# Optimization experiments

Hardware: AMD Instinct MI355X
Metric: run time of the kernel (lower is better)

Reference implementation:

```python
import jax, jax.numpy as jnp
import numpy as np

L = 64        # label_size = len(label2id)
START = 62    # label2id['START']
STOP = 63     # label2id['STOP']
T = 200000    # sequence length
NEG = -10000.0


def setup_inputs() -> dict:
    key = jax.random.key(0)
    k1, k2 = jax.random.split(key)
    lstm_feats = jax.random.normal(k1, (1, T, L), dtype=jnp.float32)
    transitions = jax.random.normal(k2, (L, L), dtype=jnp.float32)
    # CRF constructor masks: cannot transition INTO START, cannot transition FROM STOP
    transitions = transitions.at[START, :].set(NEG).at[:, STOP].set(NEG)
    return {"lstm_feats": lstm_feats, "transitions": transitions}


def reference(lstm_feats, transitions):
    # Viterbi decode, vectorized over tags; lax.scan over time replaces the
    # nested Python loops of the original (same recurrence, same math).
    feats = lstm_feats[0]  # (T, L)
    init = jnp.full((L,), NEG, dtype=lstm_feats.dtype).at[START].set(0.0)

    def step(v, feat):
        # scores[next, prev] = v[prev] + transitions[next, prev]
        scores = v[None, :] + transitions          # (L, L)
        bp = jnp.argmax(scores, axis=1).astype(jnp.int32)  # backpointers per next_tag
        v_new = jnp.max(scores, axis=1) + feat     # viterbi vars + emission
        return v_new, bp

    v, bptrs = jax.lax.scan(step, init, feats)     # bptrs: (T, L)

    terminal = v + transitions[STOP]               # (L,)
    best = jnp.argmax(terminal).astype(jnp.int32)
    path_score = terminal[best]

    # Backtrack: reverse scan emits the tag chosen at each time step, in order.
    def back(tag, bp):
        return bp[tag], tag

    _, best_path = jax.lax.scan(back, best, bptrs, reverse=True)  # (T,) int32
    return path_score, best_path
```

## Files before the change

kernel.cpp:

```cpp
#include <hip/hip_runtime.h>

#define L 64
#define TLEN 200000
#define CH 528
#define NCH 379
#define LASTLEN (TLEN - (NCH - 1) * CH)
#define MAINT 199992
#define NEGV -10000.0f
#define STARTT 62
#define STOPT 63

#define CKPT_OFF 0
#define M_OFF ((NCH + 1) * L * 4)
#define ETAG_OFF (M_OFF + NCH * L)

typedef float f32x4 __attribute__((ext_vector_type(4)));

#define WAVE_BARRIER() __asm__ volatile("s_waitcnt lgkmcnt(0)\ns_barrier" ::: "memory")
#define STEP_BARRIER() __asm__ volatile("" ::: "memory")

__global__ __launch_bounds__(256, 1) void k_forward(const float* __restrict__ feats,
                                                    const float* __restrict__ trans,
                                                    float* __restrict__ ckpt) {
    const int tid = threadIdx.x;
    const int n = tid & 63;
    const int w = tid >> 6;

    const f32x4* t4 = reinterpret_cast<const f32x4*>(trans) + n * 16 + w * 4;
    f32x4 q0 = t4[0], q1 = t4[1], q2 = t4[2], q3 = t4[3];
    __asm__ volatile("" : "+v"(q0), "+v"(q1), "+v"(q2), "+v"(q3));

    __shared__ __align__(16) float vbuf[3][L];

    vbuf[0][n] = (n == STARTT) ? 0.0f : NEGV;
    vbuf[1][n] = -INFINITY;
    vbuf[2][n] = -INFINITY;
    WAVE_BARRIER();

    float fc[6];
#pragma unroll
    for (int j = 0; j < 6; ++j) fc[j] = feats[j * L + n];

    int nextck = 0, cidx = 0;

#define FWD_STEP(RD, WR, RS, FEAT)                                            \
    do {                                                                      \
        if (w == 0) vbuf[RS][n] = -INFINITY;                                  \
        const f32x4 va0 = *reinterpret_cast<const f32x4*>(&vbuf[RD][16 * w + 0]);  \
        const f32x4 va1 = *reinterpret_cast<const f32x4*>(&vbuf[RD][16 * w + 4]);  \
        const f32x4 va2 = *reinterpret_cast<const f32x4*>(&vbuf[RD][16 * w + 8]);  \
        const f32x4 va3 = *reinterpret_cast<const f32x4*>(&vbuf[RD][16 * w + 12]); \
        const f32x4 s0 = va0 + q0, s1 = va1 + q1, s2 = va2 + q2, s3 = va3 + q3;    \
        const float m0 = fmaxf(fmaxf(s0.x, s0.y), fmaxf(s0.z, s0.w));         \
        const float m1 = fmaxf(fmaxf(s1.x, s1.y), fmaxf(s1.z, s1.w));         \
        const float m2 = fmaxf(fmaxf(s2.x, s2.y), fmaxf(s2.z, s2.w));         \
        const float m3 = fmaxf(fmaxf(s3.x, s3.y), fmaxf(s3.z, s3.w));         \
        const float cand = fmaxf(fmaxf(m0, m1), fmaxf(m2, m3)) + (FEAT);      \
        __hip_atomic_fetch_max(&vbuf[WR][n], cand, __ATOMIC_RELAXED,          \
                               __HIP_MEMORY_SCOPE_WORKGROUP);                 \
        WAVE_BARRIER();                                                       \
    } while (0)

    for (int tb = 0; tb < MAINT; tb += 6) {
        if (tb == nextck) {
            if (w == 0) ckpt[cidx * L + n] = vbuf[0][n];
            nextck += CH;
            ++cidx;
        }
        float fn_[6];
        const bool more = (tb + 6) < MAINT;
        if (more) {
#pragma unroll
            for (int j = 0; j < 6; ++j) fn_[j] = feats[(tb + 6 + j) * L + n];
        }
        FWD_STEP(0, 1, 2, fc[0]);
        FWD_STEP(1, 2, 0, fc[1]);
        FWD_STEP(2, 0, 1, fc[2]);
        FWD_STEP(0, 1, 2, fc[3]);
        FWD_STEP(1, 2, 0, fc[4]);
        FWD_STEP(2, 0, 1, fc[5]);
        if (more) {
#pragma unroll
            for (int j = 0; j < 6; ++j) fc[j] = fn_[j];
        }
    }

    float ft[8];
#pragma unroll
    for (int j = 0; j < 8; ++j) ft[j] = feats[(MAINT + j) * L + n];
    FWD_STEP(0, 1, 2, ft[0]);
    FWD_STEP(1, 2, 0, ft[1]);
    FWD_STEP(2, 0, 1, ft[2]);
    FWD_STEP(0, 1, 2, ft[3]);
    FWD_STEP(1, 2, 0, ft[4]);
    FWD_STEP(2, 0, 1, ft[5]);
    FWD_STEP(0, 1, 2, ft[6]);
    FWD_STEP(1, 2, 0, ft[7]);
    if (w == 0) ckpt[NCH * L + n] = vbuf[2][n];
#undef FWD_STEP
}

__device__ __forceinline__ void load_trow(const float* __restrict__ trans, int n, float* trow) {
#pragma unroll
    for (int i = 0; i < 16; ++i) {
        const f32x4 q = reinterpret_cast<const f32x4*>(trans)[n * 16 + i];
        trow[4 * i + 0] = q.x;
        trow[4 * i + 1] = q.y;
        trow[4 * i + 2] = q.z;
        trow[4 * i + 3] = q.w;
    }
}

__device__ __forceinline__ void replay_chunk(const float* __restrict__ feats,
                                             const float* __restrict__ ckpt,
                                             const float* trow, float* vsh,
                                             unsigned char* bpl, int c, int len, int n) {
    float vreg = ckpt[c * L + n];
    vsh[n] = vreg;
    STEP_BARRIER();
    const int base = c * CH;

    float fc[8];
#pragma unroll
    for (int j = 0; j < 8; ++j) fc[j] = feats[(base + j) * L + n];

    for (int sb = 0; sb < len; sb += 8) {
        float fn_[8];
        const bool more = (sb + 8) < len;
        if (more) {
#pragma unroll
            for (int j = 0; j < 8; ++j) fn_[j] = feats[(base + sb + 8 + j) * L + n];
        }
#pragma unroll
        for (int j = 0; j < 8; ++j) {
            float mc[4];
            int ic[4];
#pragma unroll
            for (int g = 0; g < 4; ++g) {
                float m = -INFINITY;
                int idx = g * 16;
#pragma unroll
                for (int r = 0; r < 4; ++r) {
                    const int pb = g * 16 + r * 4;
                    const f32x4 vv = *reinterpret_cast<const f32x4*>(vsh + pb);
                    const float a = vv.x + trow[pb + 0];
                    const float b = vv.y + trow[pb + 1];
                    const float cc = vv.z + trow[pb + 2];
                    const float d = vv.w + trow[pb + 3];
                    if (a > m)  { m = a;  idx = pb + 0; }
                    if (b > m)  { m = b;  idx = pb + 1; }
                    if (cc > m) { m = cc; idx = pb + 2; }
                    if (d > m)  { m = d;  idx = pb + 3; }
                }
                mc[g] = m;
                ic[g] = idx;
            }
            float m = mc[0];
            int idx = ic[0];
            if (mc[1] > m) { m = mc[1]; idx = ic[1]; }
            if (mc[2] > m) { m = mc[2]; idx = ic[2]; }
            if (mc[3] > m) { m = mc[3]; idx = ic[3]; }

            vreg = m + fc[j];
            bpl[(sb + j) * L + n] = (unsigned char)idx;
            vsh[n] = vreg;
            STEP_BARRIER();
        }
        if (more) {
#pragma unroll
            for (int j = 0; j < 8; ++j) fc[j] = fn_[j];
        }
    }
}

__global__ __launch_bounds__(64, 1) void k_maps(const float* __restrict__ feats,
                                                const float* __restrict__ trans,
                                                const float* __restrict__ ckpt,
                                                unsigned char* __restrict__ M) {
    const int c = blockIdx.x;
    const int n = threadIdx.x;
    const int len = (c == NCH - 1) ? LASTLEN : CH;

    __shared__ __align__(16) float vsh[L];
    __shared__ unsigned char bpl[CH * L];

    float trow[L];
    load_trow(trans, n, trow);
    replay_chunk(feats, ckpt, trow, vsh, bpl, c, len, n);
    __syncthreads();

    int tag = n;
    for (int s = len - 1; s >= 0; --s) tag = bpl[s * L + tag];
    M[c * L + n] = (unsigned char)tag;
}

__global__ __launch_bounds__(64, 1) void k_stitch(const float* __restrict__ trans,
                                                  const float* __restrict__ ckpt,
                                                  const unsigned char* __restrict__ M,
                                                  int* __restrict__ etag,
                                                  float* __restrict__ out) {
    const int n = threadIdx.x;
    __shared__ float tsh[L];
    __shared__ int bsh;
    __shared__ __align__(16) unsigned char msh[NCH * L];

    tsh[n] = ckpt[NCH * L + n] + trans[STOPT * L + n];
    __syncthreads();
    if (n == 0) {
        float m = tsh[0];
        int b = 0;
        for (int p = 1; p < L; ++p)
            if (tsh[p] > m) { m = tsh[p]; b = p; }
        out[0] = m;
        bsh = b;
    }
    __syncthreads();

    for (int i = n; i < (NCH * L) / 4; i += L)
        reinterpret_cast<int*>(msh)[i] = reinterpret_cast<const int*>(M)[i];
    __syncthreads();

    if (n == 0) {
        int carry = bsh;
        for (int c = NCH - 1; c >= 1; --c) {
            etag[c] = carry;
            carry = msh[c * L + carry];
        }
        etag[0] = carry;
    }
}

__global__ __launch_bounds__(64, 1) void k_emit(const float* __restrict__ feats,
                                                const float* __restrict__ trans,
                                                const float* __restrict__ ckpt,
                                                const int* __restrict__ etag,
                                                float* __restrict__ out) {
    const int c = blockIdx.x;
    const int n = threadIdx.x;
    const int len = (c == NCH - 1) ? LASTLEN : CH;

    __shared__ __align__(16) float vsh[L];
    __shared__ unsigned char bpl[CH * L];
    __shared__ unsigned char plc[CH];

    float trow[L];
    load_trow(trans, n, trow);
    replay_chunk(feats, ckpt, trow, vsh, bpl, c, len, n);
    __syncthreads();

    int tag = etag[c];
    for (int s = len - 1; s >= 0; --s) {
        if (n == 0) plc[s] = (unsigned char)tag;
        tag = bpl[s * L + tag];
    }
    __syncthreads();

    for (int i = n; i < len; i += L)
        out[1 + c * CH + i] = (float)plc[i];
}

extern "C" void kernel_launch(void* const* d_in, const int* in_sizes, int n_in,
                              void* d_out, int out_size, void* d_ws, size_t ws_size,
                              hipStream_t stream) {
    const float* feats = (const float*)d_in[0];
    const float* trans = (const float*)d_in[1];
    float* out = (float*)d_out;
    char* ws = (char*)d_ws;
    float* ckpt = (float*)(ws + CKPT_OFF);
    unsigned char* M = (unsigned char*)(ws + M_OFF);
    int* etag = (int*)(ws + ETAG_OFF);

    hipLaunchKernelGGL(k_forward, dim3(1), dim3(256), 0, stream, feats, trans, ckpt);
    hipLaunchKernelGGL(k_maps, dim3(NCH), dim3(64), 0, stream, feats, trans, ckpt, M);
    hipLaunchKernelGGL(k_stitch, dim3(1), dim3(64), 0, stream, trans, ckpt, M, etag, out);
    hipLaunchKernelGGL(k_emit, dim3(NCH), dim3(64), 0, stream, feats, trans, ckpt, etag, out);
}
```

Measured before the change: 33.07 ms.

## Run serial Viterbi forward pass in a single wave without block barriers

The forward max-plus recurrence moves from four waves that combine partial maxima through LDS atomic-max plus s_barrier to a single 64-lane wave that computes the full 64-way max per tag. The first 16 predecessors are taken with readlane broadcasts from registers and the other 48 come from LDS vector reads, reduced with v_max3. This removes the per-step workgroup barrier and the atomic, at the cost of about four times more arithmetic per lane and 64 transition values held in registers. The step unroll goes from 6 to 8, and the separate tail loop is dropped because 8 divides T.

```diff
diff --git a/kernel.cpp b/kernel.cpp
--- a/kernel.cpp
+++ b/kernel.cpp
@@ -5,7 +5,6 @@
 #define CH 528
 #define NCH 379
 #define LASTLEN (TLEN - (NCH - 1) * CH)
-#define MAINT 199992
 #define NEGV -10000.0f
 #define STARTT 62
 #define STOPT 63
@@ -16,87 +15,116 @@
 
 typedef float f32x4 __attribute__((ext_vector_type(4)));
 
-#define WAVE_BARRIER() __asm__ volatile("s_waitcnt lgkmcnt(0)\ns_barrier" ::: "memory")
 #define STEP_BARRIER() __asm__ volatile("" ::: "memory")
 
-__global__ __launch_bounds__(256, 1) void k_forward(const float* __restrict__ feats,
-                                                    const float* __restrict__ trans,
-                                                    float* __restrict__ ckpt) {
-    const int tid = threadIdx.x;
-    const int n = tid & 63;
-    const int w = tid >> 6;
-
-    const f32x4* t4 = reinterpret_cast<const f32x4*>(trans) + n * 16 + w * 4;
-    f32x4 q0 = t4[0], q1 = t4[1], q2 = t4[2], q3 = t4[3];
-    __asm__ volatile("" : "+v"(q0), "+v"(q1), "+v"(q2), "+v"(q3));
-
-    __shared__ __align__(16) float vbuf[3][L];
-
-    vbuf[0][n] = (n == STARTT) ? 0.0f : NEGV;
-    vbuf[1][n] = -INFINITY;
-    vbuf[2][n] = -INFINITY;
-    WAVE_BARRIER();
-
-    float fc[6];
-#pragma unroll
-    for (int j = 0; j < 6; ++j) fc[j] = feats[j * L + n];
+__device__ __forceinline__ float max3f(float a, float b, float c) {
+    float r;
+    __asm__("v_max3_f32 %0, %1, %2, %3" : "=v"(r) : "v"(a), "v"(b), "v"(c));
+    return r;
+}
+__device__ __forceinline__ f32x4 vmax3q(f32x4 a, f32x4 b, f32x4 c) {
+    f32x4 r;
+    r.x = max3f(a.x, b.x, c.x);
+    r.y = max3f(a.y, b.y, c.y);
+    r.z = max3f(a.z, b.z, c.z);
+    r.w = max3f(a.w, b.w, c.w);
+    return r;
+}
+
+#define QC(q, k) ((k) == 0 ? (q).x : ((k) == 1 ? (q).y : ((k) == 2 ? (q).z : (q).w)))
+
+__global__ __launch_bounds__(64, 1) void k_forward(const float* __restrict__ feats,
+                                                   const float* __restrict__ trans,
+                                                   float* __restrict__ ckpt) {
+    const int n = threadIdx.x;
+
+    f32x4 tq[16];
+#pragma unroll
+    for (int i = 0; i < 16; ++i) tq[i] = reinterpret_cast<const f32x4*>(trans)[n * 16 + i];
+
+    __shared__ __align__(16) float vsh[L];
+    const f32x4* vs4 = reinterpret_cast<const f32x4*>(vsh);
+
+    float vreg = (n == STARTT) ? 0.0f : NEGV;
+    vsh[n] = vreg;
+    STEP_BARRIER();
+
+    float fc[8];
+#pragma unroll
+    for (int j = 0; j < 8; ++j) fc[j] = feats[j * L + n];
+
+#define FWD_STEP(FEAT)                                                         \
+    do {                                                                       \
+               \
+        float h[16];                                                           \
+        _Pragma("unroll") for (int p = 0; p < 16; ++p) {                       \
+            const float vp = __int_as_float(                                   \
+                __builtin_amdgcn_readlane(__float_as_int(vreg), p));           \
+            h[p] = vp + QC(tq[p >> 2], p & 3);                                 \
+        }                                                                      \
+        const float a0 = max3f(h[0], h[1], h[2]);                              \
+        const float a1 = max3f(h[3], h[4], h[5]);                              \
+        const float a2 = max3f(h[6], h[7], h[8]);                              \
+        const float a3 = max3f(h[9], h[10], h[11]);                            \
+        const float a4 = max3f(h[12], h[13], h[14]);                           \
+        const float mh = fmaxf(max3f(a0, a1, a2), max3f(a3, a4, h[15]));       \
+              \
+        const f32x4 s4 = vs4[4] + tq[4];                                       \
+        const f32x4 s5 = vs4[5] + tq[5];                                       \
+        const f32x4 s6 = vs4[6] + tq[6];                                       \
+        const f32x4 s7 = vs4[7] + tq[7];                                       \
+        const f32x4 s8 = vs4[8] + tq[8];                                       \
+        const f32x4 s9 = vs4[9] + tq[9];                                       \
+        const f32x4 s10 = vs4[10] + tq[10];                                    \
+        const f32x4 s11 = vs4[11] + tq[11];                                    \
+        const f32x4 s12 = vs4[12] + tq[12];                                    \
+        const f32x4 s13 = vs4[13] + tq[13];                                    \
+        const f32x4 s14 = vs4[14] + tq[14];                                    \
+        const f32x4 s15 = vs4[15] + tq[15];                                    \
+        const f32x4 c0 = vmax3q(s4, s5, s6);                                   \
+        const f32x4 c1 = vmax3q(s7, s8, s9);                                   \
+        const f32x4 c2 = vmax3q(s10, s11, s12);                                \
+        const f32x4 c3 = vmax3q(s13, s14, s15);                                \
+        const f32x4 d0 = vmax3q(c0, c1, c2);                                   \
+        f32x4 e;                                                               \
+        e.x = fmaxf(d0.x, c3.x);                                               \
+        e.y = fmaxf(d0.y, c3.y);                                               \
+        e.z = fmaxf(d0.z, c3.z);                                               \
+        e.w = fmaxf(d0.w, c3.w);                                               \
+        const float m = max3f(max3f(e.x, e.y, e.z), e.w, mh);                  \
+        vreg = m + (FEAT);                                                     \
+        vsh[n] = vreg;                                                         \
+        STEP_BARRIER();                                                        \
+    } while (0)
 
     int nextck = 0, cidx = 0;
 
-#define FWD_STEP(RD, WR, RS, FEAT)                                            \
-    do {                                                                      \
-        if (w == 0) vbuf[RS][n] = -INFINITY;                                  \
-        const f32x4 va0 = *reinterpret_cast<const f32x4*>(&vbuf[RD][16 * w + 0]);  \
-        const f32x4 va1 = *reinterpret_cast<const f32x4*>(&vbuf[RD][16 * w + 4]);  \
-        const f32x4 va2 = *reinterpret_cast<const f32x4*>(&vbuf[RD][16 * w + 8]);  \
-        const f32x4 va3 = *reinterpret_cast<const f32x4*>(&vbuf[RD][16 * w + 12]); \
-        const f32x4 s0 = va0 + q0, s1 = va1 + q1, s2 = va2 + q2, s3 = va3 + q3;    \
-        const float m0 = fmaxf(fmaxf(s0.x, s0.y), fmaxf(s0.z, s0.w));         \
-        const float m1 = fmaxf(fmaxf(s1.x, s1.y), fmaxf(s1.z, s1.w));         \
-        const float m2 = fmaxf(fmaxf(s2.x, s2.y), fmaxf(s2.z, s2.w));         \
-        const float m3 = fmaxf(fmaxf(s3.x, s3.y), fmaxf(s3.z, s3.w));         \
-        const float cand = fmaxf(fmaxf(m0, m1), fmaxf(m2, m3)) + (FEAT);      \
-        __hip_atomic_fetch_max(&vbuf[WR][n], cand, __ATOMIC_RELAXED,          \
-                               __HIP_MEMORY_SCOPE_WORKGROUP);                 \
-        WAVE_BARRIER();                                                       \
-    } while (0)
-
-    for (int tb = 0; tb < MAINT; tb += 6) {
+    for (int tb = 0; tb < TLEN; tb += 8) {
         if (tb == nextck) {
-            if (w == 0) ckpt[cidx * L + n] = vbuf[0][n];
+            ckpt[cidx * L + n] = vreg;
             nextck += CH;
             ++cidx;
         }
-        float fn_[6];
-        const bool more = (tb + 6) < MAINT;
+        float fn_[8];
+        const bool more = (tb + 8) < TLEN;
         if (more) {
 #pragma unroll
-            for (int j = 0; j < 6; ++j) fn_[j] = feats[(tb + 6 + j) * L + n];
-        }
-        FWD_STEP(0, 1, 2, fc[0]);
-        FWD_STEP(1, 2, 0, fc[1]);
-        FWD_STEP(2, 0, 1, fc[2]);
-        FWD_STEP(0, 1, 2, fc[3]);
-        FWD_STEP(1, 2, 0, fc[4]);
-        FWD_STEP(2, 0, 1, fc[5]);
+            for (int j = 0; j < 8; ++j) fn_[j] = feats[(tb + 8 + j) * L + n];
+        }
+        FWD_STEP(fc[0]);
+        FWD_STEP(fc[1]);
+        FWD_STEP(fc[2]);
+        FWD_STEP(fc[3]);
+        FWD_STEP(fc[4]);
+        FWD_STEP(fc[5]);
+        FWD_STEP(fc[6]);
+        FWD_STEP(fc[7]);
         if (more) {
 #pragma unroll
-            for (int j = 0; j < 6; ++j) fc[j] = fn_[j];
-        }
-    }
-
-    float ft[8];
-#pragma unroll
-    for (int j = 0; j < 8; ++j) ft[j] = feats[(MAINT + j) * L + n];
-    FWD_STEP(0, 1, 2, ft[0]);
-    FWD_STEP(1, 2, 0, ft[1]);
-    FWD_STEP(2, 0, 1, ft[2]);
-    FWD_STEP(0, 1, 2, ft[3]);
-    FWD_STEP(1, 2, 0, ft[4]);
-    FWD_STEP(2, 0, 1, ft[5]);
-    FWD_STEP(0, 1, 2, ft[6]);
-    FWD_STEP(1, 2, 0, ft[7]);
-    if (w == 0) ckpt[NCH * L + n] = vbuf[2][n];
+            for (int j = 0; j < 8; ++j) fc[j] = fn_[j];
+        }
+    }
+    ckpt[NCH * L + n] = vreg;
 #undef FWD_STEP
 }
 
@@ -270,7 +298,7 @@
     unsigned char* M = (unsigned char*)(ws + M_OFF);
     int* etag = (int*)(ws + ETAG_OFF);
 
-    hipLaunchKernelGGL(k_forward, dim3(1), dim3(256), 0, stream, feats, trans, ckpt);
+    hipLaunchKernelGGL(k_forward, dim3(1), dim3(64), 0, stream, feats, trans, ckpt);
     hipLaunchKernelGGL(k_maps, dim3(NCH), dim3(64), 0, stream, feats, trans, ckpt, M);
     hipLaunchKernelGGL(k_stitch, dim3(1), dim3(64), 0, stream, trans, ckpt, M, etag, out);
     hipLaunchKernelGGL(k_emit, dim3(NCH), dim3(64), 0, stream, feats, trans, ckpt, etag, out);
```

After: 61.44 ms. +85.8%, slower.
